# Kernel tuning notes

Hardware: AMD Instinct MI355X
Metric: run time of the kernel (lower is better)

## Reference

```python
import jax, jax.numpy as jnp
import numpy as np

B, H, W = 16, 352, 352
EPS = 1e-7

# Directable[TL_table[i]] for i = 0..7: (dx, dy), dx=+1 shifts right, dy=+1 shifts down
# TL_table = [lower_right, down, lower_left, right, left, upper_right, up, upper_left]
SHIFTS = [(1, 1), (0, 1), (-1, 1), (1, 0), (-1, 0), (1, -1), (0, -1), (-1, -1)]


def _shift(x, dx, dy):
    # x: [B,H,W]; zero-padded translation, equivalent to the bmm against the
    # near-identity translation matrices in the original code.
    if dx == 1:
        x = jnp.pad(x, ((0, 0), (0, 0), (1, 0)))[:, :, :-1]
    elif dx == -1:
        x = jnp.pad(x, ((0, 0), (0, 0), (0, 1)))[:, :, 1:]
    if dy == 1:
        x = jnp.pad(x, ((0, 0), (1, 0), (0, 0)))[:, :-1, :]
    elif dy == -1:
        x = jnp.pad(x, ((0, 0), (0, 1), (0, 0)))[:, 1:, :]
    return x


def _bce_sum(p, t):
    p = jnp.clip(p, EPS, 1.0 - EPS)
    return -jnp.sum(t * jnp.log(p) + (1.0 - t) * jnp.log1p(-p))


def setup_inputs() -> dict:
    key = jax.random.key(0)
    k1, k2, k3 = jax.random.split(key, 3)
    c_map = jax.random.normal(k1, (B, 8, H, W), dtype=jnp.float32)
    target = jax.random.uniform(k2, (B, 1, H, W), dtype=jnp.float32)
    con_target = jax.random.randint(k3, (B, 8, H, W), 0, 2, dtype=jnp.int32)
    return {"c_map": c_map, "target": target, "con_target": con_target}


def reference(c_map, target, con_target):
    p = jax.nn.sigmoid(c_map)                      # [B,8,H,W]
    con = con_target.astype(p.dtype)
    sum_conn = jnp.sum(con, axis=1)                # [B,H,W]
    edge = ((sum_conn < 8) & (sum_conn > 0)).astype(p.dtype)

    # Bilateral voting: shifted[:, i] = shift(p[:, 7-i], direction_i)
    shifted = jnp.stack(
        [_shift(p[:, 7 - i], *SHIFTS[i]) for i in range(8)], axis=1
    )                                              # [B,8,H,W]
    vote = p * shifted                             # [B,8,H,W]

    glo_map = jnp.max(vote, axis=1)                # [B,H,W]
    pred_mask_min = jnp.min(vote, axis=1)          # [B,H,W]
    decouple = glo_map * (1.0 - edge) + (1.0 - pred_mask_min) * edge

    de_loss = _bce_sum(decouple[:, None], target)
    conmap_l = _bce_sum(p, con)
    bimap_l = _bce_sum(vote, con)
    return 0.8 * conmap_l + de_loss + 0.2 * bimap_l
```

## Files before the change

### kernel.cpp

```cpp
#include <hip/hip_runtime.h>


#define EPSF 1e-7f

constexpr int B_ = 16, H = 352, W = 352;
constexpr int HW = H * W;
constexpr int W4 = W / 4;
constexpr int RPT = 4;
constexpr int STRIPS = H / RPT;
constexpr int SPB = STRIPS * W4;
constexpr int NT = B_ * SPB;
constexpr int BLK = 256;
constexpr int NBLK = NT / BLK;

typedef float f4 __attribute__((ext_vector_type(4)));
typedef int   i4 __attribute__((ext_vector_type(4)));

__device__ __forceinline__ float rcpf(float x) { return __builtin_amdgcn_rcpf(x); }
__device__ __forceinline__ float sigf(float x) { return rcpf(1.0f + __expf(-x)); }

__device__ __forceinline__ f4 sigmoid4(f4 x) {
    f4 r;
    r.x = rcpf(1.0f + __expf(-x.x));
    r.y = rcpf(1.0f + __expf(-x.y));
    r.z = rcpf(1.0f + __expf(-x.z));
    r.w = rcpf(1.0f + __expf(-x.w));
    return r;
}
__device__ __forceinline__ f4 max4(f4 a, f4 b) {
    f4 r; r.x=fmaxf(a.x,b.x); r.y=fmaxf(a.y,b.y); r.z=fmaxf(a.z,b.z); r.w=fmaxf(a.w,b.w); return r;
}
__device__ __forceinline__ f4 min4(f4 a, f4 b) {
    f4 r; r.x=fminf(a.x,b.x); r.y=fminf(a.y,b.y); r.z=fminf(a.z,b.z); r.w=fminf(a.w,b.w); return r;
}
__device__ __forceinline__ f4 sel4(i4 q, f4 a, f4 b) {
    f4 r; r.x=q.x?a.x:b.x; r.y=q.y?a.y:b.y; r.z=q.z?a.z:b.z; r.w=q.w?a.w:b.w; return r;
}
__device__ __forceinline__ f4 ld4(const float* p) { return *(const f4*)p; }
__device__ __forceinline__ i4 ldi4(const int* p)  { return *(const i4*)p; }

__device__ __forceinline__ f4 shiftR4(f4 p, float fixL, bool isLane0) {
    float left = __shfl_up(p.w, 1, 64);
    if (isLane0) left = fixL;
    f4 r; r.x = left; r.y = p.x; r.z = p.y; r.w = p.z; return r;
}
__device__ __forceinline__ f4 shiftL4(f4 p, float fixR, bool isLane63) {
    float right = __shfl_down(p.x, 1, 64);
    if (isLane63) right = fixR;
    f4 r; r.x = p.y; r.y = p.z; r.z = p.w; r.w = right; return r;
}

__device__ __forceinline__ float finish_pixel(float glo, float pmin, int sc,
                                              float t, float cp, float ba, float bb) {
    const float edge = (sc < 8 && sc > 0) ? 1.0f : 0.0f;
    float dec = glo * (1.0f - edge) + (1.0f - pmin) * edge;
    dec = fminf(fmaxf(dec, EPSF), 1.0f - EPSF);
    const float de = -(t * __logf(dec) + (1.0f - t) * __logf(1.0f - dec));
    return de - 0.8f * __logf(cp) - 0.2f * (__logf(ba) + __logf(bb));
}

__global__ __launch_bounds__(BLK) void bicon_r13_main(
    const float* __restrict__ c_map,
    const float* __restrict__ target,
    const int*   __restrict__ con,
    float* __restrict__ ws)
{
    const int tid   = blockIdx.x * BLK + threadIdx.x;
    const int b     = tid / SPB;
    const int rem   = tid - b * SPB;
    const int strip = rem / W4;
    const int xq    = rem - strip * W4;
    const int x0    = xq * 4;
    const int y0    = strip * RPT;
    const int lane  = threadIdx.x & 63;

    const float* __restrict__ cmb = c_map + (size_t)b * 8 * HW;
    const int*   __restrict__ cnb = con   + (size_t)b * 8 * HW;
    const float* __restrict__ tb  = target + (size_t)b * HW;

    const float lm = (xq == 0)      ? 0.0f : 1.0f;
    const float rm = (xq == W4 - 1) ? 0.0f : 1.0f;

    const int ypr = (y0 > 0) ? y0 - 1 : 0;
    f4 pp5 = sigmoid4(ld4(cmb + 5 * HW + ypr * W + x0));
    f4 pp6 = sigmoid4(ld4(cmb + 6 * HW + ypr * W + x0));
    f4 pp7 = sigmoid4(ld4(cmb + 7 * HW + ypr * W + x0));
    f4 p0 = sigmoid4(ld4(cmb + 0 * HW + y0 * W + x0));
    f4 p1 = sigmoid4(ld4(cmb + 1 * HW + y0 * W + x0));
    f4 p2 = sigmoid4(ld4(cmb + 2 * HW + y0 * W + x0));
    f4 p3 = sigmoid4(ld4(cmb + 3 * HW + y0 * W + x0));
    f4 p4 = sigmoid4(ld4(cmb + 4 * HW + y0 * W + x0));
    f4 p5 = sigmoid4(ld4(cmb + 5 * HW + y0 * W + x0));
    f4 p6 = sigmoid4(ld4(cmb + 6 * HW + y0 * W + x0));
    f4 p7 = sigmoid4(ld4(cmb + 7 * HW + y0 * W + x0));

    float part = 0.0f;

    #pragma unroll
    for (int r = 0; r < RPT; ++r) {
        const bool fullPrefetch = (r != RPT - 1);
        const int y  = y0 + r;
        const int yn = (y + 1 < H) ? y + 1 : y;
        const int ypc = (y > 0) ? y - 1 : 0;
        const float* cyn = cmb + yn * W + x0;

        const f4 cn0 = ld4(cyn + 0 * HW);
        const f4 cn1 = ld4(cyn + 1 * HW);
        const f4 cn2 = ld4(cyn + 2 * HW);
        f4 cn3{}, cn4{}, cn5{}, cn6{}, cn7{};
        if (fullPrefetch) {
            cn3 = ld4(cyn + 3 * HW);
            cn4 = ld4(cyn + 4 * HW);
            cn5 = ld4(cyn + 5 * HW);
            cn6 = ld4(cyn + 6 * HW);
            cn7 = ld4(cyn + 7 * HW);
        }
        const int* qy = cnb + y * W + x0;
        const i4 q0 = ldi4(qy + 0 * HW);
        const i4 q1 = ldi4(qy + 1 * HW);
        const i4 q2 = ldi4(qy + 2 * HW);
        const i4 q3 = ldi4(qy + 3 * HW);
        const i4 q4 = ldi4(qy + 4 * HW);
        const i4 q5 = ldi4(qy + 5 * HW);
        const i4 q6 = ldi4(qy + 6 * HW);
        const i4 q7 = ldi4(qy + 7 * HW);
        const f4 t4 = ld4(tb + y * W + x0);

        float fA = 0.f, fB = 0.f, fC = 0.f, fD = 0.f, fE = 0.f, fF = 0.f;
        if (lane == 0) {
            const int xl = (xq == 0) ? x0 : x0 - 1;
            fA = sigf(cmb[7 * HW + ypc * W + xl]);
            fB = sigf(cmb[4 * HW + y   * W + xl]);
            fC = sigf(cmb[2 * HW + yn  * W + xl]);
        } else if (lane == 63) {
            const int xr = (xq == W4 - 1) ? x0 + 3 : x0 + 4;
            fD = sigf(cmb[5 * HW + ypc * W + xr]);
            fE = sigf(cmb[3 * HW + y   * W + xr]);
            fF = sigf(cmb[0 * HW + yn  * W + xr]);
        }

        const f4 pn0 = sigmoid4(cn0);
        const f4 pn1 = sigmoid4(cn1);
        const f4 pn2 = sigmoid4(cn2);

        const float tm = (y == 0)     ? 0.0f : 1.0f;
        const float bm = (y == H - 1) ? 0.0f : 1.0f;

        const f4 s0 = shiftR4(pp7, fA, lane == 0);
        const f4 s1 = pp6;
        const f4 s2 = shiftL4(pp5, fD, lane == 63);
        const f4 s3 = shiftR4(p4,  fB, lane == 0);
        const f4 s4 = shiftL4(p3,  fE, lane == 63);
        const f4 s5 = shiftR4(pn2, fC, lane == 0);
        const f4 s6 = pn1;
        const f4 s7 = shiftL4(pn0, fF, lane == 63);

        f4 conprod = {1.f,1.f,1.f,1.f};
        f4 biA     = {1.f,1.f,1.f,1.f};
        f4 biB     = {1.f,1.f,1.f,1.f};
        f4 glo     = {-1e30f,-1e30f,-1e30f,-1e30f};
        f4 pmin    = { 1e30f, 1e30f, 1e30f, 1e30f};

#define DIR(P, Q, S, DX, RMASK, BI) {                                         \
        f4 s = (S);                                                           \
        s *= (RMASK);                                                         \
        if ((DX) == 1)  s.x *= lm;                                            \
        if ((DX) == -1) s.w *= rm;                                            \
        const f4 v = (P) * s;                                                 \
        glo  = max4(glo,  v);                                                 \
        pmin = min4(pmin, v);                                                 \
        conprod *= sel4((Q), (P), 1.0f - (P));                                \
        BI *= sel4((Q), max4(v, (f4){EPSF,EPSF,EPSF,EPSF}), 1.0f - v);        \
    }
        DIR(p0, q0, s0,  1, tm, biA)
        DIR(p1, q1, s1,  0, tm, biA)
        DIR(p2, q2, s2, -1, tm, biA)
        DIR(p3, q3, s3,  1, 1.0f, biA)
        DIR(p4, q4, s4, -1, 1.0f, biB)
        DIR(p5, q5, s5,  1, bm, biB)
        DIR(p6, q6, s6,  0, bm, biB)
        DIR(p7, q7, s7, -1, bm, biB)
#undef DIR

        const i4 sc = q0 + q1 + q2 + q3 + q4 + q5 + q6 + q7;

        part += finish_pixel(glo.x, pmin.x, sc.x, t4.x, conprod.x, biA.x, biB.x)
              + finish_pixel(glo.y, pmin.y, sc.y, t4.y, conprod.y, biA.y, biB.y)
              + finish_pixel(glo.z, pmin.z, sc.z, t4.z, conprod.z, biA.z, biB.z)
              + finish_pixel(glo.w, pmin.w, sc.w, t4.w, conprod.w, biA.w, biB.w);

        pp5 = p5; pp6 = p6; pp7 = p7;
        p0 = pn0; p1 = pn1; p2 = pn2;
        if (fullPrefetch) {
            p3 = sigmoid4(cn3);
            p4 = sigmoid4(cn4);
            p5 = sigmoid4(cn5);
            p6 = sigmoid4(cn6);
            p7 = sigmoid4(cn7);
        }
    }

    #pragma unroll
    for (int off = 32; off > 0; off >>= 1)
        part += __shfl_down(part, off, 64);

    __shared__ float wsum[4];
    const int wid = threadIdx.x >> 6;
    if (lane == 0) wsum[wid] = part;
    __syncthreads();
    if (threadIdx.x == 0) {
        ws[blockIdx.x] = wsum[0] + wsum[1] + wsum[2] + wsum[3];
    }
}

__global__ __launch_bounds__(256) void bicon_r13_reduce(
    const float* __restrict__ ws, float* __restrict__ out)
{
    float s = 0.0f;
    for (int i = threadIdx.x; i < NBLK; i += 256) s += ws[i];
    #pragma unroll
    for (int off = 32; off > 0; off >>= 1)
        s += __shfl_down(s, off, 64);
    __shared__ float wsum[4];
    const int lane = threadIdx.x & 63;
    const int wid  = threadIdx.x >> 6;
    if (lane == 0) wsum[wid] = s;
    __syncthreads();
    if (threadIdx.x == 0) out[0] = wsum[0] + wsum[1] + wsum[2] + wsum[3];
}

extern "C" void kernel_launch(void* const* d_in, const int* in_sizes, int n_in,
                              void* d_out, int out_size, void* d_ws, size_t ws_size,
                              hipStream_t stream) {
    const float* c_map  = (const float*)d_in[0];
    const float* target = (const float*)d_in[1];
    const int*   con    = (const int*)d_in[2];
    float* out = (float*)d_out;
    float* ws  = (float*)d_ws;

    bicon_r13_main<<<NBLK, BLK, 0, stream>>>(c_map, target, con, ws);
    bicon_r13_reduce<<<1, 256, 0, stream>>>(ws, out);
}
```

Before: 167.4 us.

## Halve rows per thread, hand-unroll two rows, and cap registers for occupancy

```diff
diff --git a/kernel.cpp b/kernel.cpp
--- a/kernel.cpp
+++ b/kernel.cpp
@@ -6,7 +6,7 @@
 constexpr int B_ = 16, H = 352, W = 352;
 constexpr int HW = H * W;
 constexpr int W4 = W / 4;
-constexpr int RPT = 4;
+constexpr int RPT = 2;
 constexpr int STRIPS = H / RPT;
 constexpr int SPB = STRIPS * W4;
 constexpr int NT = B_ * SPB;
@@ -59,7 +59,56 @@
     return de - 0.8f * __logf(cp) - 0.2f * (__logf(ba) + __logf(bb));
 }
 
-__global__ __launch_bounds__(BLK) void bicon_r13_main(
+#define DIR(P, Q, S, DX, RMASK, BI) {                                         \
+        f4 s_ = (S);                                                          \
+        s_ *= (RMASK);                                                        \
+        if ((DX) == 1)  s_.x *= lm;                                           \
+        if ((DX) == -1) s_.w *= rm;                                           \
+        const f4 v = (P) * s_;                                                \
+        glo  = max4(glo,  v);                                                 \
+        pmin = min4(pmin, v);                                                 \
+        conprod *= sel4((Q), (P), 1.0f - (P));                                \
+        BI *= sel4((Q), max4(v, (f4){EPSF,EPSF,EPSF,EPSF}), 1.0f - v);        \
+    }
+
+#define ROW(P0,P1,P2,P3,P4,P5,P6,P7, S0,S1,S2,S3,S4,S5,S6,S7, QY, TP, TM, BM) { \
+        const int* qy_ = (QY);                                                \
+        f4 conprod = {1.f,1.f,1.f,1.f};                                       \
+        f4 biA     = {1.f,1.f,1.f,1.f};                                       \
+        f4 biB     = {1.f,1.f,1.f,1.f};                                       \
+        f4 glo     = {-1e30f,-1e30f,-1e30f,-1e30f};                           \
+        f4 pmin    = { 1e30f, 1e30f, 1e30f, 1e30f};                           \
+        i4 sc;                                                                \
+        {                                                                     \
+            const i4 q0 = ldi4(qy_ + 0 * HW);                                 \
+            const i4 q1 = ldi4(qy_ + 1 * HW);                                 \
+            const i4 q2 = ldi4(qy_ + 2 * HW);                                 \
+            const i4 q3 = ldi4(qy_ + 3 * HW);                                 \
+            DIR(P0, q0, S0,  1, TM,   biA)                                    \
+            DIR(P1, q1, S1,  0, TM,   biA)                                    \
+            DIR(P2, q2, S2, -1, TM,   biA)                                    \
+            DIR(P3, q3, S3,  1, 1.0f, biA)                                    \
+            sc = q0 + q1 + q2 + q3;                                           \
+        }                                                                     \
+        {                                                                     \
+            const i4 q4 = ldi4(qy_ + 4 * HW);                                 \
+            const i4 q5 = ldi4(qy_ + 5 * HW);                                 \
+            const i4 q6 = ldi4(qy_ + 6 * HW);                                 \
+            const i4 q7 = ldi4(qy_ + 7 * HW);                                 \
+            DIR(P4, q4, S4, -1, 1.0f, biB)                                    \
+            DIR(P5, q5, S5,  1, BM,   biB)                                    \
+            DIR(P6, q6, S6,  0, BM,   biB)                                    \
+            DIR(P7, q7, S7, -1, BM,   biB)                                    \
+            sc += q4 + q5 + q6 + q7;                                          \
+        }                                                                     \
+        const f4 t4 = ld4(TP);                                                \
+        part += finish_pixel(glo.x, pmin.x, sc.x, t4.x, conprod.x, biA.x, biB.x) \
+              + finish_pixel(glo.y, pmin.y, sc.y, t4.y, conprod.y, biA.y, biB.y) \
+              + finish_pixel(glo.z, pmin.z, sc.z, t4.z, conprod.z, biA.z, biB.z) \
+              + finish_pixel(glo.w, pmin.w, sc.w, t4.w, conprod.w, biA.w, biB.w); \
+    }
+
+__global__ __launch_bounds__(BLK, 4) void bicon_r14_main(
     const float* __restrict__ c_map,
     const float* __restrict__ target,
     const int*   __restrict__ con,
@@ -72,6 +121,7 @@
     const int xq    = rem - strip * W4;
     const int x0    = xq * 4;
     const int y0    = strip * RPT;
+    const int y1    = y0 + 1;
     const int lane  = threadIdx.x & 63;
 
     const float* __restrict__ cmb = c_map + (size_t)b * 8 * HW;
@@ -80,124 +130,83 @@
 
     const float lm = (xq == 0)      ? 0.0f : 1.0f;
     const float rm = (xq == W4 - 1) ? 0.0f : 1.0f;
-
-    const int ypr = (y0 > 0) ? y0 - 1 : 0;
-    f4 pp5 = sigmoid4(ld4(cmb + 5 * HW + ypr * W + x0));
-    f4 pp6 = sigmoid4(ld4(cmb + 6 * HW + ypr * W + x0));
-    f4 pp7 = sigmoid4(ld4(cmb + 7 * HW + ypr * W + x0));
-    f4 p0 = sigmoid4(ld4(cmb + 0 * HW + y0 * W + x0));
-    f4 p1 = sigmoid4(ld4(cmb + 1 * HW + y0 * W + x0));
-    f4 p2 = sigmoid4(ld4(cmb + 2 * HW + y0 * W + x0));
-    f4 p3 = sigmoid4(ld4(cmb + 3 * HW + y0 * W + x0));
-    f4 p4 = sigmoid4(ld4(cmb + 4 * HW + y0 * W + x0));
-    f4 p5 = sigmoid4(ld4(cmb + 5 * HW + y0 * W + x0));
-    f4 p6 = sigmoid4(ld4(cmb + 6 * HW + y0 * W + x0));
-    f4 p7 = sigmoid4(ld4(cmb + 7 * HW + y0 * W + x0));
+    const int ypr = (y0 > 0)    ? y0 - 1 : 0;
+    const int yn2 = (y1 + 1 < H) ? y1 + 1 : y1;
+    const int xl  = (xq == 0)      ? x0     : x0 - 1;
+    const int xr  = (xq == W4 - 1) ? x0 + 3 : x0 + 4;
 
     float part = 0.0f;
 
-    #pragma unroll
-    for (int r = 0; r < RPT; ++r) {
-        const bool fullPrefetch = (r != RPT - 1);
-        const int y  = y0 + r;
-        const int yn = (y + 1 < H) ? y + 1 : y;
-        const int ypc = (y > 0) ? y - 1 : 0;
-        const float* cyn = cmb + yn * W + x0;
-
-        const f4 cn0 = ld4(cyn + 0 * HW);
-        const f4 cn1 = ld4(cyn + 1 * HW);
-        const f4 cn2 = ld4(cyn + 2 * HW);
-        f4 cn3{}, cn4{}, cn5{}, cn6{}, cn7{};
-        if (fullPrefetch) {
-            cn3 = ld4(cyn + 3 * HW);
-            cn4 = ld4(cyn + 4 * HW);
-            cn5 = ld4(cyn + 5 * HW);
-            cn6 = ld4(cyn + 6 * HW);
-            cn7 = ld4(cyn + 7 * HW);
-        }
-        const int* qy = cnb + y * W + x0;
-        const i4 q0 = ldi4(qy + 0 * HW);
-        const i4 q1 = ldi4(qy + 1 * HW);
-        const i4 q2 = ldi4(qy + 2 * HW);
-        const i4 q3 = ldi4(qy + 3 * HW);
-        const i4 q4 = ldi4(qy + 4 * HW);
-        const i4 q5 = ldi4(qy + 5 * HW);
-        const i4 q6 = ldi4(qy + 6 * HW);
-        const i4 q7 = ldi4(qy + 7 * HW);
-        const f4 t4 = ld4(tb + y * W + x0);
-
+    f4 a5 = sigmoid4(ld4(cmb + 5 * HW + ypr * W + x0));
+    f4 a6 = sigmoid4(ld4(cmb + 6 * HW + ypr * W + x0));
+    f4 a7 = sigmoid4(ld4(cmb + 7 * HW + ypr * W + x0));
+    f4 b0 = sigmoid4(ld4(cmb + 0 * HW + y0 * W + x0));
+    f4 b1 = sigmoid4(ld4(cmb + 1 * HW + y0 * W + x0));
+    f4 b2 = sigmoid4(ld4(cmb + 2 * HW + y0 * W + x0));
+    f4 b3 = sigmoid4(ld4(cmb + 3 * HW + y0 * W + x0));
+    f4 b4 = sigmoid4(ld4(cmb + 4 * HW + y0 * W + x0));
+    f4 b5 = sigmoid4(ld4(cmb + 5 * HW + y0 * W + x0));
+    f4 b6 = sigmoid4(ld4(cmb + 6 * HW + y0 * W + x0));
+    f4 b7 = sigmoid4(ld4(cmb + 7 * HW + y0 * W + x0));
+    f4 c0 = sigmoid4(ld4(cmb + 0 * HW + y1 * W + x0));
+    f4 c1 = sigmoid4(ld4(cmb + 1 * HW + y1 * W + x0));
+    f4 c2 = sigmoid4(ld4(cmb + 2 * HW + y1 * W + x0));
+
+    {
         float fA = 0.f, fB = 0.f, fC = 0.f, fD = 0.f, fE = 0.f, fF = 0.f;
         if (lane == 0) {
-            const int xl = (xq == 0) ? x0 : x0 - 1;
-            fA = sigf(cmb[7 * HW + ypc * W + xl]);
-            fB = sigf(cmb[4 * HW + y   * W + xl]);
-            fC = sigf(cmb[2 * HW + yn  * W + xl]);
+            fA = sigf(cmb[7 * HW + ypr * W + xl]);
+            fB = sigf(cmb[4 * HW + y0  * W + xl]);
+            fC = sigf(cmb[2 * HW + y1  * W + xl]);
         } else if (lane == 63) {
-            const int xr = (xq == W4 - 1) ? x0 + 3 : x0 + 4;
-            fD = sigf(cmb[5 * HW + ypc * W + xr]);
-            fE = sigf(cmb[3 * HW + y   * W + xr]);
-            fF = sigf(cmb[0 * HW + yn  * W + xr]);
+            fD = sigf(cmb[5 * HW + ypr * W + xr]);
+            fE = sigf(cmb[3 * HW + y0  * W + xr]);
+            fF = sigf(cmb[0 * HW + y1  * W + xr]);
         }
-
-        const f4 pn0 = sigmoid4(cn0);
-        const f4 pn1 = sigmoid4(cn1);
-        const f4 pn2 = sigmoid4(cn2);
-
-        const float tm = (y == 0)     ? 0.0f : 1.0f;
-        const float bm = (y == H - 1) ? 0.0f : 1.0f;
-
-        const f4 s0 = shiftR4(pp7, fA, lane == 0);
-        const f4 s1 = pp6;
-        const f4 s2 = shiftL4(pp5, fD, lane == 63);
-        const f4 s3 = shiftR4(p4,  fB, lane == 0);
-        const f4 s4 = shiftL4(p3,  fE, lane == 63);
-        const f4 s5 = shiftR4(pn2, fC, lane == 0);
-        const f4 s6 = pn1;
-        const f4 s7 = shiftL4(pn0, fF, lane == 63);
-
-        f4 conprod = {1.f,1.f,1.f,1.f};
-        f4 biA     = {1.f,1.f,1.f,1.f};
-        f4 biB     = {1.f,1.f,1.f,1.f};
-        f4 glo     = {-1e30f,-1e30f,-1e30f,-1e30f};
-        f4 pmin    = { 1e30f, 1e30f, 1e30f, 1e30f};
-
-#define DIR(P, Q, S, DX, RMASK, BI) {                                         \
-        f4 s = (S);                                                           \
-        s *= (RMASK);                                                         \
-        if ((DX) == 1)  s.x *= lm;                                            \
-        if ((DX) == -1) s.w *= rm;                                            \
-        const f4 v = (P) * s;                                                 \
-        glo  = max4(glo,  v);                                                 \
-        pmin = min4(pmin, v);                                                 \
-        conprod *= sel4((Q), (P), 1.0f - (P));                                \
-        BI *= sel4((Q), max4(v, (f4){EPSF,EPSF,EPSF,EPSF}), 1.0f - v);        \
-    }
-        DIR(p0, q0, s0,  1, tm, biA)
-        DIR(p1, q1, s1,  0, tm, biA)
-        DIR(p2, q2, s2, -1, tm, biA)
-        DIR(p3, q3, s3,  1, 1.0f, biA)
-        DIR(p4, q4, s4, -1, 1.0f, biB)
-        DIR(p5, q5, s5,  1, bm, biB)
-        DIR(p6, q6, s6,  0, bm, biB)
-        DIR(p7, q7, s7, -1, bm, biB)
-#undef DIR
-
-        const i4 sc = q0 + q1 + q2 + q3 + q4 + q5 + q6 + q7;
-
-        part += finish_pixel(glo.x, pmin.x, sc.x, t4.x, conprod.x, biA.x, biB.x)
-              + finish_pixel(glo.y, pmin.y, sc.y, t4.y, conprod.y, biA.y, biB.y)
-              + finish_pixel(glo.z, pmin.z, sc.z, t4.z, conprod.z, biA.z, biB.z)
-              + finish_pixel(glo.w, pmin.w, sc.w, t4.w, conprod.w, biA.w, biB.w);
-
-        pp5 = p5; pp6 = p6; pp7 = p7;
-        p0 = pn0; p1 = pn1; p2 = pn2;
-        if (fullPrefetch) {
-            p3 = sigmoid4(cn3);
-            p4 = sigmoid4(cn4);
-            p5 = sigmoid4(cn5);
-            p6 = sigmoid4(cn6);
-            p7 = sigmoid4(cn7);
+        const float tm = (y0 == 0) ? 0.0f : 1.0f;
+        const f4 s0 = shiftR4(a7, fA, lane == 0);
+        const f4 s1 = a6;
+        const f4 s2 = shiftL4(a5, fD, lane == 63);
+        const f4 s3 = shiftR4(b4, fB, lane == 0);
+        const f4 s4 = shiftL4(b3, fE, lane == 63);
+        const f4 s5 = shiftR4(c2, fC, lane == 0);
+        const f4 s6 = c1;
+        const f4 s7 = shiftL4(c0, fF, lane == 63);
+        ROW(b0,b1,b2,b3,b4,b5,b6,b7, s0,s1,s2,s3,s4,s5,s6,s7,
+            cnb + y0 * W + x0, tb + y0 * W + x0, tm, 1.0f)
+    }
+
+    {
+        f4 d3 = sigmoid4(ld4(cmb + 3 * HW + y1 * W + x0));
+        f4 d4 = sigmoid4(ld4(cmb + 4 * HW + y1 * W + x0));
+        f4 d5 = sigmoid4(ld4(cmb + 5 * HW + y1 * W + x0));
+        f4 d6 = sigmoid4(ld4(cmb + 6 * HW + y1 * W + x0));
+        f4 d7 = sigmoid4(ld4(cmb + 7 * HW + y1 * W + x0));
+        f4 e0 = sigmoid4(ld4(cmb + 0 * HW + yn2 * W + x0));
+        f4 e1 = sigmoid4(ld4(cmb + 1 * HW + yn2 * W + x0));
+        f4 e2 = sigmoid4(ld4(cmb + 2 * HW + yn2 * W + x0));
+
+        float fA = 0.f, fB = 0.f, fC = 0.f, fD = 0.f, fE = 0.f, fF = 0.f;
+        if (lane == 0) {
+            fA = sigf(cmb[7 * HW + y0  * W + xl]);
+            fB = sigf(cmb[4 * HW + y1  * W + xl]);
+            fC = sigf(cmb[2 * HW + yn2 * W + xl]);
+        } else if (lane == 63) {
+            fD = sigf(cmb[5 * HW + y0  * W + xr]);
+            fE = sigf(cmb[3 * HW + y1  * W + xr]);
+            fF = sigf(cmb[0 * HW + yn2 * W + xr]);
         }
+        const float bm = (y1 == H - 1) ? 0.0f : 1.0f;
+        const f4 s0 = shiftR4(b7, fA, lane == 0);
+        const f4 s1 = b6;
+        const f4 s2 = shiftL4(b5, fD, lane == 63);
+        const f4 s3 = shiftR4(d4, fB, lane == 0);
+        const f4 s4 = shiftL4(d3, fE, lane == 63);
+        const f4 s5 = shiftR4(e2, fC, lane == 0);
+        const f4 s6 = e1;
+        const f4 s7 = shiftL4(e0, fF, lane == 63);
+        ROW(c0,c1,c2,d3,d4,d5,d6,d7, s0,s1,s2,s3,s4,s5,s6,s7,
+            cnb + y1 * W + x0, tb + y1 * W + x0, 1.0f, bm)
     }
 
     #pragma unroll
@@ -213,7 +222,7 @@
     }
 }
 
-__global__ __launch_bounds__(256) void bicon_r13_reduce(
+__global__ __launch_bounds__(256) void bicon_r14_reduce(
     const float* __restrict__ ws, float* __restrict__ out)
 {
     float s = 0.0f;
@@ -238,6 +247,6 @@
     float* out = (float*)d_out;
     float* ws  = (float*)d_ws;
 
-    bicon_r13_main<<<NBLK, BLK, 0, stream>>>(c_map, target, con, ws);
-    bicon_r13_reduce<<<1, 256, 0, stream>>>(ws, out);
-}
+    bicon_r14_main<<<NBLK, BLK, 0, stream>>>(c_map, target, con, ws);
+    bicon_r14_reduce<<<1, 256, 0, stream>>>(ws, out);
+}
```

Result: slower. 176.6 us (+5.5%).
